# Performance work log

Measured on AMD Instinct MI355X. Metric: run time of the kernel, lower is better.

## Reference

```python
import jax, jax.numpy as jnp
import numpy as np

B, L, D, DFF = 4, 4096, 1024, 4096
EPS = 1e-6

def _rmsnorm(x, w):
    return x * jax.lax.rsqrt(jnp.mean(x * x, axis=-1, keepdims=True) + EPS) * w

def setup_inputs() -> dict:
    key = jax.random.key(0)
    ks = jax.random.split(key, 16)
    s = 1.0 / np.sqrt(D)
    sf = 1.0 / np.sqrt(DFF)
    return {
        "x": jax.random.normal(ks[0], (B, L, D), jnp.float32),
        # QuasiLSTM gate linears, stored [in, out]; y = x @ W + b
        "w_forget": jax.random.normal(ks[1], (D, D), jnp.float32) * s,
        "b_forget": jnp.zeros((D,), jnp.float32),
        "w_input": jax.random.normal(ks[2], (D, D), jnp.float32) * s,
        "b_input": jnp.zeros((D,), jnp.float32),
        "w_igate": jax.random.normal(ks[3], (D, D), jnp.float32) * s,
        "b_igate": jnp.zeros((D,), jnp.float32),
        "w_ogate": jax.random.normal(ks[4], (D, D), jnp.float32) * s,
        "b_ogate": jnp.zeros((D,), jnp.float32),
        "h0": jax.random.normal(ks[5], (D,), jnp.float32),  # last_hidden_init
        "norm1_w": jnp.ones((D,), jnp.float32),
        "norm2_w": jnp.ones((D,), jnp.float32),
        # FFN SwiGLU
        "w_fc": jax.random.normal(ks[6], (D, DFF), jnp.float32) * s,
        "b_fc": jnp.zeros((DFF,), jnp.float32),
        "w_fc_act": jax.random.normal(ks[7], (D, DFF), jnp.float32) * s,
        "b_fc_act": jnp.zeros((DFF,), jnp.float32),
        "w_out": jax.random.normal(ks[8], (DFF, D), jnp.float32) * sf,
        "b_out": jnp.zeros((D,), jnp.float32),
    }

def reference(x, w_forget, b_forget, w_input, b_input, w_igate, b_igate,
              w_ogate, b_ogate, h0, norm1_w, norm2_w,
              w_fc, b_fc, w_fc_act, b_fc_act, w_out, b_out):
    # --- QuasiLSTM branch (pre-norm residual) ---
    x_res = x
    xn = _rmsnorm(x, norm1_w)                                   # [B,L,D]
    forget = jax.nn.sigmoid(xn @ w_forget + b_forget)           # a_t
    inp = jnp.tanh(xn @ w_input + b_input) * jax.nn.sigmoid(xn @ w_igate + b_igate)  # b_t
    # Linear recurrence h_t = a_t * h_{t-1} + b_t, h_0 = 0 (inner chunk),
    # computed as an associative scan over the length axis.
    def comb(left, right):
        a_l, b_l = left
        a_r, b_r = right
        return (a_l * a_r, b_l * a_r + b_r)
    _, h_inner = jax.lax.associative_scan(comb, (forget, inp), axis=1)
    # cross-chunk contribution from last_hidden_init
    h = h_inner + h0[None, None, :] * jnp.cumprod(forget, axis=1)
    y = jnp.tanh(h) * jax.nn.sigmoid(xn @ w_ogate + b_ogate)
    x1 = y + x_res  # dropout p=0 -> identity
    # --- FFN SwiGLU branch ---
    xn2 = _rmsnorm(x1, norm2_w)
    hff = (xn2 @ w_fc + b_fc) * jax.nn.silu(xn2 @ w_fc_act + b_fc_act)
    out = hff @ w_out + b_out
    return out + x1
```

## Files before the change

### kernel.cpp

```cpp
#include <hip/hip_runtime.h>
#include <math.h>
#include <stdint.h>

static constexpr int Bb  = 4;
static constexpr int Ll  = 4096;
static constexpr int Dd  = 1024;
static constexpr int DFF = 4096;
static constexpr int Mm  = Bb * Ll;
static constexpr int CH  = 64;
static constexpr int CS  = Ll / CH;
static constexpr float EPS = 1e-6f;

typedef __attribute__((ext_vector_type(8))) short short8;
typedef __attribute__((ext_vector_type(4))) float floatx4;
typedef __attribute__((ext_vector_type(4))) unsigned short us4;

__device__ __forceinline__ float sigmoidf_(float v) { return 1.0f / (1.0f + __expf(-v)); }
__device__ __forceinline__ ushort f2bf(float f) {
    union { float f; uint32_t u; } v; v.f = f;
    return (ushort)((v.u + 0x7FFFu + ((v.u >> 16) & 1u)) >> 16);
}
__device__ __forceinline__ float bf2f(ushort h) {
    union { uint32_t u; float f; } v; v.u = (uint32_t)h << 16; return v.f;
}

__device__ __forceinline__ void gload16(const ushort* g, ushort* l) {
    __builtin_amdgcn_global_load_lds(
        (const __attribute__((address_space(1))) uint32_t*)g,
        (__attribute__((address_space(3))) uint32_t*)l, 16, 0, 0);
}

__device__ __forceinline__ void stage128x32(const ushort* __restrict__ src, int ld,
                                            int r0, int k0, ushort* lds, int tid)
{
    #pragma unroll
    for (int h = 0; h < 2; ++h) {
        int c  = tid + h * 256;
        int m  = c >> 2;
        int kb = (c & 3) ^ ((m >> 1) & 3);
        gload16(src + (size_t)(r0 + m) * ld + k0 + kb * 8, lds + c * 8);
    }
}

__global__ __launch_bounds__(256, 2) void mfma_gemm_sigmoid(
    const ushort* __restrict__ A, const ushort* __restrict__ Wt,
    const float* __restrict__ bias, ushort* __restrict__ C,
    int K, int ldC)
{
    __shared__ ushort As[128 * 32];
    __shared__ ushort Bs[128 * 32];
    int tid = threadIdx.x;
    int m0 = blockIdx.y * 128, n0 = blockIdx.x * 128;
    int wave = tid >> 6, lane = tid & 63;
    int wm = (wave >> 1) * 64, wn = (wave & 1) * 64;
    int fr = lane & 15, q = lane >> 4;
    int sw = (q ^ ((fr >> 1) & 3)) * 8;

    floatx4 acc[4][4] = {};

    for (int k0 = 0; k0 < K; k0 += 32) {
        stage128x32(A,  K, m0, k0, As, tid);
        stage128x32(Wt, K, n0, k0, Bs, tid);
        __syncthreads();
        short8 a[4], b[4];
        #pragma unroll
        for (int mi = 0; mi < 4; ++mi)
            a[mi] = *(const short8*)&As[(wm + mi * 16 + fr) * 32 + sw];
        #pragma unroll
        for (int ni = 0; ni < 4; ++ni)
            b[ni] = *(const short8*)&Bs[(wn + ni * 16 + fr) * 32 + sw];
        #pragma unroll
        for (int mi = 0; mi < 4; ++mi)
            #pragma unroll
            for (int ni = 0; ni < 4; ++ni)
                acc[mi][ni] = __builtin_amdgcn_mfma_f32_16x16x32_bf16(
                    a[mi], b[ni], acc[mi][ni], 0, 0, 0);
        __syncthreads();
    }

    #pragma unroll
    for (int ni = 0; ni < 4; ++ni) {
        int col = n0 + wn + ni * 16 + fr;
        float bsv = bias[col];
        #pragma unroll
        for (int mi = 0; mi < 4; ++mi)
            #pragma unroll
            for (int r = 0; r < 4; ++r) {
                int row = m0 + wm + mi * 16 + q * 4 + r;
                C[(size_t)row * ldC + col] = f2bf(sigmoidf_(acc[mi][ni][r] + bsv));
            }
    }
}

__global__ __launch_bounds__(256, 2) void mfma_gemm_dual(
    const ushort* __restrict__ A, const ushort* __restrict__ W1t,
    const float* __restrict__ b1, const ushort* __restrict__ W2t,
    const float* __restrict__ b2, ushort* __restrict__ C,
    int K, int ldC, int mode)
{
    __shared__ ushort As[128 * 32];
    __shared__ ushort B1s[128 * 32];
    __shared__ ushort B2s[128 * 32];
    int tid = threadIdx.x;
    int m0 = blockIdx.y * 128, n0 = blockIdx.x * 128;
    int wave = tid >> 6, lane = tid & 63;
    int wm = (wave >> 1) * 64, wn = (wave & 1) * 64;
    int fr = lane & 15, q = lane >> 4;
    int sw = (q ^ ((fr >> 1) & 3)) * 8;

    floatx4 acc1[4][4] = {};
    floatx4 acc2[4][4] = {};

    for (int k0 = 0; k0 < K; k0 += 32) {
        stage128x32(A,   K, m0, k0, As,  tid);
        stage128x32(W1t, K, n0, k0, B1s, tid);
        stage128x32(W2t, K, n0, k0, B2s, tid);
        __syncthreads();
        short8 a[4], b[4], c[4];
        #pragma unroll
        for (int mi = 0; mi < 4; ++mi)
            a[mi] = *(const short8*)&As[(wm + mi * 16 + fr) * 32 + sw];
        #pragma unroll
        for (int ni = 0; ni < 4; ++ni) {
            b[ni] = *(const short8*)&B1s[(wn + ni * 16 + fr) * 32 + sw];
            c[ni] = *(const short8*)&B2s[(wn + ni * 16 + fr) * 32 + sw];
        }
        #pragma unroll
        for (int mi = 0; mi < 4; ++mi)
            #pragma unroll
            for (int ni = 0; ni < 4; ++ni) {
                acc1[mi][ni] = __builtin_amdgcn_mfma_f32_16x16x32_bf16(
                    a[mi], b[ni], acc1[mi][ni], 0, 0, 0);
                acc2[mi][ni] = __builtin_amdgcn_mfma_f32_16x16x32_bf16(
                    a[mi], c[ni], acc2[mi][ni], 0, 0, 0);
            }
        __syncthreads();
    }

    #pragma unroll
    for (int ni = 0; ni < 4; ++ni) {
        int col = n0 + wn + ni * 16 + fr;
        float b1v = b1[col], b2v = b2[col];
        #pragma unroll
        for (int mi = 0; mi < 4; ++mi)
            #pragma unroll
            for (int r = 0; r < 4; ++r) {
                int row = m0 + wm + mi * 16 + q * 4 + r;
                float z1 = acc1[mi][ni][r] + b1v;
                float z2 = acc2[mi][ni][r] + b2v;
                float v = (mode == 0) ? tanhf(z1) * sigmoidf_(z2)
                                      : z1 * z2 * sigmoidf_(z2);
                C[(size_t)row * ldC + col] = f2bf(v);
            }
    }
}

__global__ __launch_bounds__(256, 2) void mfma_gemm_residual(
    const ushort* __restrict__ A, const ushort* __restrict__ Wt,
    const float* __restrict__ bias, float* __restrict__ C,
    int K, int ldC)
{
    __shared__ ushort As[128 * 32];
    __shared__ ushort Bs[128 * 32];
    int tid = threadIdx.x;
    int m0 = blockIdx.y * 128, n0 = blockIdx.x * 128;
    int wave = tid >> 6, lane = tid & 63;
    int wm = (wave >> 1) * 64, wn = (wave & 1) * 64;
    int fr = lane & 15, q = lane >> 4;
    int sw = (q ^ ((fr >> 1) & 3)) * 8;

    floatx4 acc[4][4] = {};

    for (int k0 = 0; k0 < K; k0 += 32) {
        stage128x32(A,  K, m0, k0, As, tid);
        stage128x32(Wt, K, n0, k0, Bs, tid);
        __syncthreads();
        short8 a[4], b[4];
        #pragma unroll
        for (int mi = 0; mi < 4; ++mi)
            a[mi] = *(const short8*)&As[(wm + mi * 16 + fr) * 32 + sw];
        #pragma unroll
        for (int ni = 0; ni < 4; ++ni)
            b[ni] = *(const short8*)&Bs[(wn + ni * 16 + fr) * 32 + sw];
        #pragma unroll
        for (int mi = 0; mi < 4; ++mi)
            #pragma unroll
            for (int ni = 0; ni < 4; ++ni)
                acc[mi][ni] = __builtin_amdgcn_mfma_f32_16x16x32_bf16(
                    a[mi], b[ni], acc[mi][ni], 0, 0, 0);
        __syncthreads();
    }

    #pragma unroll
    for (int ni = 0; ni < 4; ++ni) {
        int col = n0 + wn + ni * 16 + fr;
        float bsv = bias[col];
        #pragma unroll
        for (int mi = 0; mi < 4; ++mi)
            #pragma unroll
            for (int r = 0; r < 4; ++r) {
                int row = m0 + wm + mi * 16 + q * 4 + r;
                size_t idx = (size_t)row * ldC + col;
                C[idx] = acc[mi][ni][r] + bsv + C[idx];
            }
    }
}

__global__ __launch_bounds__(256) void transpose_cast_kernel(
    const float* __restrict__ W, ushort* __restrict__ Wt, int K, int N)
{
    __shared__ float t[32][33];
    int lx = threadIdx.x & 31, ly = threadIdx.x >> 5;
    int n = blockIdx.x * 32 + lx;
    #pragma unroll
    for (int i = 0; i < 4; ++i) {
        int k = blockIdx.y * 32 + ly + i * 8;
        t[ly + i * 8][lx] = W[(size_t)k * N + n];
    }
    __syncthreads();
    int k2 = blockIdx.y * 32 + lx;
    #pragma unroll
    for (int i = 0; i < 4; ++i) {
        int n2 = blockIdx.x * 32 + ly + i * 8;
        Wt[(size_t)n2 * K + k2] = f2bf(t[lx][ly + i * 8]);
    }
}

__global__ __launch_bounds__(256) void rmsnorm_bf16_kernel(
    const float* __restrict__ x, const float* __restrict__ w,
    ushort* __restrict__ o)
{
    int row = blockIdx.x;
    int tid = threadIdx.x;
    float4 v = ((const float4*)(x + (size_t)row * Dd))[tid];
    float ss = v.x*v.x + v.y*v.y + v.z*v.z + v.w*v.w;
    #pragma unroll
    for (int off = 32; off > 0; off >>= 1) ss += __shfl_down(ss, off, 64);
    __shared__ float red[4];
    if ((tid & 63) == 0) red[tid >> 6] = ss;
    __syncthreads();
    float scale = rsqrtf((red[0] + red[1] + red[2] + red[3]) * (1.0f / Dd) + EPS);
    float4 wv = ((const float4*)w)[tid];
    us4 ov;
    ov.x = f2bf(v.x * scale * wv.x);
    ov.y = f2bf(v.y * scale * wv.y);
    ov.z = f2bf(v.z * scale * wv.z);
    ov.w = f2bf(v.w * scale * wv.w);
    *(us4*)&o[(size_t)row * Dd + tid * 4] = ov;
}

__global__ __launch_bounds__(256) void scan_pass1(
    const ushort* __restrict__ Ga, const ushort* __restrict__ Gb,
    float* __restrict__ P, float* __restrict__ Hend)
{
    int d = blockIdx.x * 256 + threadIdx.x;
    int c = blockIdx.y, b = blockIdx.z;
    size_t base = ((size_t)b * Ll + (size_t)c * CS) * Dd + d;
    float p = 1.0f, h = 0.0f;
    for (int t = 0; t < CS; ++t) {
        size_t i = base + (size_t)t * Dd;
        float aa = bf2f(Ga[i]);
        float bb = bf2f(Gb[i]);
        p *= aa;
        h = aa * h + bb;
    }
    size_t o = ((size_t)b * CH + c) * Dd + d;
    P[o] = p;
    Hend[o] = h;
}

__global__ __launch_bounds__(256) void scan_pass2(
    const float* __restrict__ P, const float* __restrict__ Hend,
    const float* __restrict__ h0, float* __restrict__ Carry)
{
    int idx = blockIdx.x * 256 + threadIdx.x;
    int b = idx / Dd, d = idx % Dd;
    float carry = h0[d];
    for (int c = 0; c < CH; ++c) {
        size_t o = ((size_t)b * CH + c) * Dd + d;
        Carry[o] = carry;
        carry = P[o] * carry + Hend[o];
    }
}

__global__ __launch_bounds__(256) void scan_pass3_fused(
    const ushort* __restrict__ Ga, const ushort* __restrict__ Gb,
    const ushort* __restrict__ Gog, const float* __restrict__ Carry,
    const float* __restrict__ x, float* __restrict__ x1)
{
    int d = blockIdx.x * 256 + threadIdx.x;
    int c = blockIdx.y, b = blockIdx.z;
    size_t base = ((size_t)b * Ll + (size_t)c * CS) * Dd + d;
    float h = Carry[((size_t)b * CH + c) * Dd + d];
    for (int t = 0; t < CS; ++t) {
        size_t i = base + (size_t)t * Dd;
        float aa = bf2f(Ga[i]);
        float bb = bf2f(Gb[i]);
        h = aa * h + bb;
        x1[i] = tanhf(h) * bf2f(Gog[i]) + x[i];
    }
}

extern "C" void kernel_launch(void* const* d_in, const int* in_sizes, int n_in,
                              void* d_out, int out_size, void* d_ws, size_t ws_size,
                              hipStream_t stream)
{
    const float* x        = (const float*)d_in[0];
    const float* w_forget = (const float*)d_in[1];
    const float* b_forget = (const float*)d_in[2];
    const float* w_input  = (const float*)d_in[3];
    const float* b_input  = (const float*)d_in[4];
    const float* w_igate  = (const float*)d_in[5];
    const float* b_igate  = (const float*)d_in[6];
    const float* w_ogate  = (const float*)d_in[7];
    const float* b_ogate  = (const float*)d_in[8];
    const float* h0       = (const float*)d_in[9];
    const float* norm1_w  = (const float*)d_in[10];
    const float* norm2_w  = (const float*)d_in[11];
    const float* w_fc     = (const float*)d_in[12];
    const float* b_fc     = (const float*)d_in[13];
    const float* w_fc_act = (const float*)d_in[14];
    const float* b_fc_act = (const float*)d_in[15];
    const float* w_out    = (const float*)d_in[16];
    const float* b_out    = (const float*)d_in[17];
    float* out = (float*)d_out;

    char* ws = (char*)d_ws;
    const size_t MB = 1ull << 20;
    ushort* wtF   = (ushort*)(ws + 0 * MB);
    ushort* wtI   = (ushort*)(ws + 2 * MB);
    ushort* wtG   = (ushort*)(ws + 4 * MB);
    ushort* wtO   = (ushort*)(ws + 6 * MB);
    ushort* wtFC  = (ushort*)(ws + 8 * MB);
    ushort* wtFCA = (ushort*)(ws + 16 * MB);
    ushort* wtOUT = (ushort*)(ws + 24 * MB);
    ushort* xnb   = (ushort*)(ws + 32 * MB);
    ushort* Ga    = (ushort*)(ws + 64 * MB);
    ushort* Gb    = (ushort*)(ws + 96 * MB);
    ushort* Gog   = (ushort*)(ws + 128 * MB);
    ushort* hff   = (ushort*)(ws + 64 * MB);
    float*  P     = (float*)(ws + 192 * MB);
    float*  Hend  = (float*)(ws + 193 * MB);
    float*  Carry = (float*)(ws + 194 * MB);

    transpose_cast_kernel<<<dim3(Dd/32, Dd/32), 256, 0, stream>>>(w_forget, wtF,  Dd, Dd);
    transpose_cast_kernel<<<dim3(Dd/32, Dd/32), 256, 0, stream>>>(w_input,  wtI,  Dd, Dd);
    transpose_cast_kernel<<<dim3(Dd/32, Dd/32), 256, 0, stream>>>(w_igate,  wtG,  Dd, Dd);
    transpose_cast_kernel<<<dim3(Dd/32, Dd/32), 256, 0, stream>>>(w_ogate,  wtO,  Dd, Dd);
    transpose_cast_kernel<<<dim3(DFF/32, Dd/32), 256, 0, stream>>>(w_fc,     wtFC,  Dd, DFF);
    transpose_cast_kernel<<<dim3(DFF/32, Dd/32), 256, 0, stream>>>(w_fc_act, wtFCA, Dd, DFF);
    transpose_cast_kernel<<<dim3(Dd/32, DFF/32), 256, 0, stream>>>(w_out,    wtOUT, DFF, Dd);

    rmsnorm_bf16_kernel<<<Mm, 256, 0, stream>>>(x, norm1_w, xnb);

    dim3 gg(Dd / 128, Mm / 128);
    mfma_gemm_sigmoid<<<gg, 256, 0, stream>>>(xnb, wtF, b_forget, Ga, Dd, Dd);
    mfma_gemm_dual<<<gg, 256, 0, stream>>>(xnb, wtI, b_input, wtG, b_igate,
                                           Gb, Dd, Dd, 0);
    mfma_gemm_sigmoid<<<gg, 256, 0, stream>>>(xnb, wtO, b_ogate, Gog, Dd, Dd);

    dim3 sg(Dd / 256, CH, Bb);
    scan_pass1<<<sg, 256, 0, stream>>>(Ga, Gb, P, Hend);
    scan_pass2<<<(Bb * Dd) / 256, 256, 0, stream>>>(P, Hend, h0, Carry);
    scan_pass3_fused<<<sg, 256, 0, stream>>>(Ga, Gb, Gog, Carry, x, out);

    rmsnorm_bf16_kernel<<<Mm, 256, 0, stream>>>(out, norm2_w, xnb);

    dim3 gf(DFF / 128, Mm / 128);
    mfma_gemm_dual<<<gf, 256, 0, stream>>>(xnb, wtFC, b_fc, wtFCA, b_fc_act,
                                           hff, Dd, DFF, 1);

    dim3 go(Dd / 128, Mm / 128);
    mfma_gemm_residual<<<go, 256, 0, stream>>>(hff, wtOUT, b_out, out, DFF, Dd);
}
```

Measured before the change: 1.022 ms.

## Merge gate GEMMs into one dual GEMM and fuse second RMSNorm into scan

The four gate projections now run as a single dual-B GEMM over 2048 output columns: [input|forget] against [igate|ogate]. The epilogue branches by column to write Gb, Ga and Gog. The scan passes switch to one block per chunk covering the full model dimension with 4-wide vector loads, and the final scan pass also computes the second RMSNorm through a block reduction, which removes a separate norm kernel and a reread of x1. tanhf is replaced with an exp-based fast tanh, and the four gate weight transposes are merged into one launch. The trade-offs are fewer blocks in the scan kernels, two barriers per timestep in pass 3, and slightly lower accuracy from the fast tanh.

```diff
diff --git a/kernel.cpp b/kernel.cpp
--- a/kernel.cpp
+++ b/kernel.cpp
@@ -16,6 +16,9 @@
 typedef __attribute__((ext_vector_type(4))) unsigned short us4;
 
 __device__ __forceinline__ float sigmoidf_(float v) { return 1.0f / (1.0f + __expf(-v)); }
+__device__ __forceinline__ float fast_tanh(float x) {
+    return 2.0f / (1.0f + __expf(-2.0f * x)) - 1.0f;
+}
 __device__ __forceinline__ ushort f2bf(float f) {
     union { float f; uint32_t u; } v; v.f = f;
     return (ushort)((v.u + 0x7FFFu + ((v.u >> 16) & 1u)) >> 16);
@@ -42,61 +45,13 @@
     }
 }
 
-__global__ __launch_bounds__(256, 2) void mfma_gemm_sigmoid(
-    const ushort* __restrict__ A, const ushort* __restrict__ Wt,
-    const float* __restrict__ bias, ushort* __restrict__ C,
-    int K, int ldC)
-{
-    __shared__ ushort As[128 * 32];
-    __shared__ ushort Bs[128 * 32];
-    int tid = threadIdx.x;
-    int m0 = blockIdx.y * 128, n0 = blockIdx.x * 128;
-    int wave = tid >> 6, lane = tid & 63;
-    int wm = (wave >> 1) * 64, wn = (wave & 1) * 64;
-    int fr = lane & 15, q = lane >> 4;
-    int sw = (q ^ ((fr >> 1) & 3)) * 8;
-
-    floatx4 acc[4][4] = {};
-
-    for (int k0 = 0; k0 < K; k0 += 32) {
-        stage128x32(A,  K, m0, k0, As, tid);
-        stage128x32(Wt, K, n0, k0, Bs, tid);
-        __syncthreads();
-        short8 a[4], b[4];
-        #pragma unroll
-        for (int mi = 0; mi < 4; ++mi)
-            a[mi] = *(const short8*)&As[(wm + mi * 16 + fr) * 32 + sw];
-        #pragma unroll
-        for (int ni = 0; ni < 4; ++ni)
-            b[ni] = *(const short8*)&Bs[(wn + ni * 16 + fr) * 32 + sw];
-        #pragma unroll
-        for (int mi = 0; mi < 4; ++mi)
-            #pragma unroll
-            for (int ni = 0; ni < 4; ++ni)
-                acc[mi][ni] = __builtin_amdgcn_mfma_f32_16x16x32_bf16(
-                    a[mi], b[ni], acc[mi][ni], 0, 0, 0);
-        __syncthreads();
-    }
-
-    #pragma unroll
-    for (int ni = 0; ni < 4; ++ni) {
-        int col = n0 + wn + ni * 16 + fr;
-        float bsv = bias[col];
-        #pragma unroll
-        for (int mi = 0; mi < 4; ++mi)
-            #pragma unroll
-            for (int r = 0; r < 4; ++r) {
-                int row = m0 + wm + mi * 16 + q * 4 + r;
-                C[(size_t)row * ldC + col] = f2bf(sigmoidf_(acc[mi][ni][r] + bsv));
-            }
-    }
-}
-
-__global__ __launch_bounds__(256, 2) void mfma_gemm_dual(
+__global__ __launch_bounds__(256, 2) void mfma_gemm_gates(
     const ushort* __restrict__ A, const ushort* __restrict__ W1t,
-    const float* __restrict__ b1, const ushort* __restrict__ W2t,
-    const float* __restrict__ b2, ushort* __restrict__ C,
-    int K, int ldC, int mode)
+    const ushort* __restrict__ W2t,
+    const float* __restrict__ b_input, const float* __restrict__ b_forget,
+    const float* __restrict__ b_igate, const float* __restrict__ b_ogate,
+    ushort* __restrict__ Ga, ushort* __restrict__ Gb, ushort* __restrict__ Gog,
+    int K)
 {
     __shared__ ushort As[128 * 32];
     __shared__ ushort B1s[128 * 32];
@@ -140,28 +95,43 @@
     #pragma unroll
     for (int ni = 0; ni < 4; ++ni) {
         int col = n0 + wn + ni * 16 + fr;
-        float b1v = b1[col], b2v = b2[col];
-        #pragma unroll
-        for (int mi = 0; mi < 4; ++mi)
-            #pragma unroll
-            for (int r = 0; r < 4; ++r) {
-                int row = m0 + wm + mi * 16 + q * 4 + r;
-                float z1 = acc1[mi][ni][r] + b1v;
-                float z2 = acc2[mi][ni][r] + b2v;
-                float v = (mode == 0) ? tanhf(z1) * sigmoidf_(z2)
-                                      : z1 * z2 * sigmoidf_(z2);
-                C[(size_t)row * ldC + col] = f2bf(v);
-            }
-    }
-}
-
-__global__ __launch_bounds__(256, 2) void mfma_gemm_residual(
-    const ushort* __restrict__ A, const ushort* __restrict__ Wt,
-    const float* __restrict__ bias, float* __restrict__ C,
+        if (col < 1024) {
+            float b1v = b_input[col], b2v = b_igate[col];
+            #pragma unroll
+            for (int mi = 0; mi < 4; ++mi)
+                #pragma unroll
+                for (int r = 0; r < 4; ++r) {
+                    int row = m0 + wm + mi * 16 + q * 4 + r;
+                    float z1 = acc1[mi][ni][r] + b1v;
+                    float z2 = acc2[mi][ni][r] + b2v;
+                    Gb[(size_t)row * Dd + col] = f2bf(fast_tanh(z1) * sigmoidf_(z2));
+                }
+        } else {
+            int c2 = col - 1024;
+            float b1v = b_forget[c2], b2v = b_ogate[c2];
+            #pragma unroll
+            for (int mi = 0; mi < 4; ++mi)
+                #pragma unroll
+                for (int r = 0; r < 4; ++r) {
+                    int row = m0 + wm + mi * 16 + q * 4 + r;
+                    float z1 = acc1[mi][ni][r] + b1v;
+                    float z2 = acc2[mi][ni][r] + b2v;
+                    Ga[(size_t)row * Dd + c2]  = f2bf(sigmoidf_(z1));
+                    Gog[(size_t)row * Dd + c2] = f2bf(sigmoidf_(z2));
+                }
+        }
+    }
+}
+
+__global__ __launch_bounds__(256, 2) void mfma_gemm_swiglu(
+    const ushort* __restrict__ A, const ushort* __restrict__ W1t,
+    const float* __restrict__ b1, const ushort* __restrict__ W2t,
+    const float* __restrict__ b2, ushort* __restrict__ C,
     int K, int ldC)
 {
     __shared__ ushort As[128 * 32];
-    __shared__ ushort Bs[128 * 32];
+    __shared__ ushort B1s[128 * 32];
+    __shared__ ushort B2s[128 * 32];
     int tid = threadIdx.x;
     int m0 = blockIdx.y * 128, n0 = blockIdx.x * 128;
     int wave = tid >> 6, lane = tid & 63;
@@ -169,6 +139,65 @@
     int fr = lane & 15, q = lane >> 4;
     int sw = (q ^ ((fr >> 1) & 3)) * 8;
 
+    floatx4 acc1[4][4] = {};
+    floatx4 acc2[4][4] = {};
+
+    for (int k0 = 0; k0 < K; k0 += 32) {
+        stage128x32(A,   K, m0, k0, As,  tid);
+        stage128x32(W1t, K, n0, k0, B1s, tid);
+        stage128x32(W2t, K, n0, k0, B2s, tid);
+        __syncthreads();
+        short8 a[4], b[4], c[4];
+        #pragma unroll
+        for (int mi = 0; mi < 4; ++mi)
+            a[mi] = *(const short8*)&As[(wm + mi * 16 + fr) * 32 + sw];
+        #pragma unroll
+        for (int ni = 0; ni < 4; ++ni) {
+            b[ni] = *(const short8*)&B1s[(wn + ni * 16 + fr) * 32 + sw];
+            c[ni] = *(const short8*)&B2s[(wn + ni * 16 + fr) * 32 + sw];
+        }
+        #pragma unroll
+        for (int mi = 0; mi < 4; ++mi)
+            #pragma unroll
+            for (int ni = 0; ni < 4; ++ni) {
+                acc1[mi][ni] = __builtin_amdgcn_mfma_f32_16x16x32_bf16(
+                    a[mi], b[ni], acc1[mi][ni], 0, 0, 0);
+                acc2[mi][ni] = __builtin_amdgcn_mfma_f32_16x16x32_bf16(
+                    a[mi], c[ni], acc2[mi][ni], 0, 0, 0);
+            }
+        __syncthreads();
+    }
+
+    #pragma unroll
+    for (int ni = 0; ni < 4; ++ni) {
+        int col = n0 + wn + ni * 16 + fr;
+        float b1v = b1[col], b2v = b2[col];
+        #pragma unroll
+        for (int mi = 0; mi < 4; ++mi)
+            #pragma unroll
+            for (int r = 0; r < 4; ++r) {
+                int row = m0 + wm + mi * 16 + q * 4 + r;
+                float z1 = acc1[mi][ni][r] + b1v;
+                float z2 = acc2[mi][ni][r] + b2v;
+                C[(size_t)row * ldC + col] = f2bf(z1 * z2 * sigmoidf_(z2));
+            }
+    }
+}
+
+__global__ __launch_bounds__(256, 2) void mfma_gemm_residual(
+    const ushort* __restrict__ A, const ushort* __restrict__ Wt,
+    const float* __restrict__ bias, float* __restrict__ C,
+    int K, int ldC)
+{
+    __shared__ ushort As[128 * 32];
+    __shared__ ushort Bs[128 * 32];
+    int tid = threadIdx.x;
+    int m0 = blockIdx.y * 128, n0 = blockIdx.x * 128;
+    int wave = tid >> 6, lane = tid & 63;
+    int wm = (wave >> 1) * 64, wn = (wave & 1) * 64;
+    int fr = lane & 15, q = lane >> 4;
+    int sw = (q ^ ((fr >> 1) & 3)) * 8;
+
     floatx4 acc[4][4] = {};
 
     for (int k0 = 0; k0 < K; k0 += 32) {
@@ -223,6 +252,32 @@
     for (int i = 0; i < 4; ++i) {
         int n2 = blockIdx.x * 32 + ly + i * 8;
         Wt[(size_t)n2 * K + k2] = f2bf(t[lx][ly + i * 8]);
+    }
+}
+
+__global__ __launch_bounds__(256) void transpose_cast_gates(
+    const float* __restrict__ w_i, const float* __restrict__ w_f,
+    const float* __restrict__ w_g, const float* __restrict__ w_o,
+    ushort* __restrict__ W1t, ushort* __restrict__ W2t)
+{
+    int z = blockIdx.z;
+    const float* W = (z == 0) ? w_i : (z == 1) ? w_f : (z == 2) ? w_g : w_o;
+    ushort* Wt = (z == 0) ? W1t : (z == 1) ? W1t + (size_t)1024 * Dd
+               : (z == 2) ? W2t : W2t + (size_t)1024 * Dd;
+    __shared__ float t[32][33];
+    int lx = threadIdx.x & 31, ly = threadIdx.x >> 5;
+    int n = blockIdx.x * 32 + lx;
+    #pragma unroll
+    for (int i = 0; i < 4; ++i) {
+        int k = blockIdx.y * 32 + ly + i * 8;
+        t[ly + i * 8][lx] = W[(size_t)k * Dd + n];
+    }
+    __syncthreads();
+    int k2 = blockIdx.y * 32 + lx;
+    #pragma unroll
+    for (int i = 0; i < 4; ++i) {
+        int n2 = blockIdx.x * 32 + ly + i * 8;
+        Wt[(size_t)n2 * Dd + k2] = f2bf(t[lx][ly + i * 8]);
     }
 }
 
@@ -253,20 +308,26 @@
     const ushort* __restrict__ Ga, const ushort* __restrict__ Gb,
     float* __restrict__ P, float* __restrict__ Hend)
 {
-    int d = blockIdx.x * 256 + threadIdx.x;
-    int c = blockIdx.y, b = blockIdx.z;
-    size_t base = ((size_t)b * Ll + (size_t)c * CS) * Dd + d;
-    float p = 1.0f, h = 0.0f;
+    int tid = threadIdx.x;
+    int c = blockIdx.x, b = blockIdx.y;
+    size_t base = ((size_t)b * Ll + (size_t)c * CS) * Dd + tid * 4;
+    float p[4] = {1.f, 1.f, 1.f, 1.f};
+    float h[4] = {};
+    #pragma unroll 4
     for (int t = 0; t < CS; ++t) {
-        size_t i = base + (size_t)t * Dd;
-        float aa = bf2f(Ga[i]);
-        float bb = bf2f(Gb[i]);
-        p *= aa;
-        h = aa * h + bb;
-    }
-    size_t o = ((size_t)b * CH + c) * Dd + d;
-    P[o] = p;
-    Hend[o] = h;
+        us4 av = *(const us4*)&Ga[base + (size_t)t * Dd];
+        us4 bv = *(const us4*)&Gb[base + (size_t)t * Dd];
+        #pragma unroll
+        for (int j = 0; j < 4; ++j) {
+            float aa = bf2f(av[j]);
+            float bb = bf2f(bv[j]);
+            p[j] *= aa;
+            h[j] = aa * h[j] + bb;
+        }
+    }
+    size_t o = ((size_t)b * CH + c) * Dd + tid * 4;
+    *(float4*)&P[o]    = make_float4(p[0], p[1], p[2], p[3]);
+    *(float4*)&Hend[o] = make_float4(h[0], h[1], h[2], h[3]);
 }
 
 __global__ __launch_bounds__(256) void scan_pass2(
@@ -283,21 +344,48 @@
     }
 }
 
-__global__ __launch_bounds__(256) void scan_pass3_fused(
+__global__ __launch_bounds__(256) void scan_pass3_norm(
     const ushort* __restrict__ Ga, const ushort* __restrict__ Gb,
     const ushort* __restrict__ Gog, const float* __restrict__ Carry,
-    const float* __restrict__ x, float* __restrict__ x1)
-{
-    int d = blockIdx.x * 256 + threadIdx.x;
-    int c = blockIdx.y, b = blockIdx.z;
-    size_t base = ((size_t)b * Ll + (size_t)c * CS) * Dd + d;
-    float h = Carry[((size_t)b * CH + c) * Dd + d];
+    const float* __restrict__ x, const float* __restrict__ norm2w,
+    float* __restrict__ x1, ushort* __restrict__ xnb)
+{
+    int tid = threadIdx.x;
+    int c = blockIdx.x, b = blockIdx.y;
+    size_t base = ((size_t)b * Ll + (size_t)c * CS) * Dd + tid * 4;
+    float4 h4 = *(const float4*)&Carry[((size_t)b * CH + c) * Dd + tid * 4];
+    float h[4] = {h4.x, h4.y, h4.z, h4.w};
+    float4 w4 = ((const float4*)norm2w)[tid];
+    float wv[4] = {w4.x, w4.y, w4.z, w4.w};
+    __shared__ float red[4];
+
     for (int t = 0; t < CS; ++t) {
         size_t i = base + (size_t)t * Dd;
-        float aa = bf2f(Ga[i]);
-        float bb = bf2f(Gb[i]);
-        h = aa * h + bb;
-        x1[i] = tanhf(h) * bf2f(Gog[i]) + x[i];
+        us4 av = *(const us4*)&Ga[i];
+        us4 bv = *(const us4*)&Gb[i];
+        us4 gv = *(const us4*)&Gog[i];
+        float4 xv = *(const float4*)&x[i];
+        float xs[4] = {xv.x, xv.y, xv.z, xv.w};
+        float v[4];
+        #pragma unroll
+        for (int j = 0; j < 4; ++j) {
+            float aa = bf2f(av[j]);
+            float bb = bf2f(bv[j]);
+            h[j] = aa * h[j] + bb;
+            v[j] = fast_tanh(h[j]) * bf2f(gv[j]) + xs[j];
+        }
+        *(float4*)&x1[i] = make_float4(v[0], v[1], v[2], v[3]);
+        float ss = v[0]*v[0] + v[1]*v[1] + v[2]*v[2] + v[3]*v[3];
+        #pragma unroll
+        for (int off = 32; off > 0; off >>= 1) ss += __shfl_down(ss, off, 64);
+        if ((tid & 63) == 0) red[tid >> 6] = ss;
+        __syncthreads();
+        float scale = rsqrtf((red[0] + red[1] + red[2] + red[3]) * (1.0f / Dd) + EPS);
+        us4 ov;
+        #pragma unroll
+        for (int j = 0; j < 4; ++j) ov[j] = f2bf(v[j] * scale * wv[j]);
+        *(us4*)&xnb[i] = ov;
+        __syncthreads();
     }
 }
 
@@ -327,10 +415,8 @@
 
     char* ws = (char*)d_ws;
     const size_t MB = 1ull << 20;
-    ushort* wtF   = (ushort*)(ws + 0 * MB);
-    ushort* wtI   = (ushort*)(ws + 2 * MB);
-    ushort* wtG   = (ushort*)(ws + 4 * MB);
-    ushort* wtO   = (ushort*)(ws + 6 * MB);
+    ushort* wtG1  = (ushort*)(ws + 0 * MB);
+    ushort* wtG2  = (ushort*)(ws + 4 * MB);
     ushort* wtFC  = (ushort*)(ws + 8 * MB);
     ushort* wtFCA = (ushort*)(ws + 16 * MB);
     ushort* wtOUT = (ushort*)(ws + 24 * MB);
@@ -343,32 +429,28 @@
     float*  Hend  = (float*)(ws + 193 * MB);
     float*  Carry = (float*)(ws + 194 * MB);
 
-    transpose_cast_kernel<<<dim3(Dd/32, Dd/32), 256, 0, stream>>>(w_forget, wtF,  Dd, Dd);
-    transpose_cast_kernel<<<dim3(Dd/32, Dd/32), 256, 0, stream>>>(w_input,  wtI,  Dd, Dd);
-    transpose_cast_kernel<<<dim3(Dd/32, Dd/32), 256, 0, stream>>>(w_igate,  wtG,  Dd, Dd);
-    transpose_cast_kernel<<<dim3(Dd/32, Dd/32), 256, 0, stream>>>(w_ogate,  wtO,  Dd, Dd);
+    transpose_cast_gates<<<dim3(32, 32, 4), 256, 0, stream>>>(
+        w_input, w_forget, w_igate, w_ogate, wtG1, wtG2);
     transpose_cast_kernel<<<dim3(DFF/32, Dd/32), 256, 0, stream>>>(w_fc,     wtFC,  Dd, DFF);
     transpose_cast_kernel<<<dim3(DFF/32, Dd/32), 256, 0, stream>>>(w_fc_act, wtFCA, Dd, DFF);
     transpose_cast_kernel<<<dim3(Dd/32, DFF/32), 256, 0, stream>>>(w_out,    wtOUT, DFF, Dd);
 
     rmsnorm_bf16_kernel<<<Mm, 256, 0, stream>>>(x, norm1_w, xnb);
 
-    dim3 gg(Dd / 128, Mm / 128);
-    mfma_gemm_sigmoid<<<gg, 256, 0, stream>>>(xnb, wtF, b_forget, Ga, Dd, Dd);
-    mfma_gemm_dual<<<gg, 256, 0, stream>>>(xnb, wtI, b_input, wtG, b_igate,
-                                           Gb, Dd, Dd, 0);
-    mfma_gemm_sigmoid<<<gg, 256, 0, stream>>>(xnb, wtO, b_ogate, Gog, Dd, Dd);
-
-    dim3 sg(Dd / 256, CH, Bb);
+    dim3 gg(2048 / 128, Mm / 128);
+    mfma_gemm_gates<<<gg, 256, 0, stream>>>(xnb, wtG1, wtG2,
+                                            b_input, b_forget, b_igate, b_ogate,
+                                            Ga, Gb, Gog, Dd);
+
+    dim3 sg(CH, Bb);
     scan_pass1<<<sg, 256, 0, stream>>>(Ga, Gb, P, Hend);
     scan_pass2<<<(Bb * Dd) / 256, 256, 0, stream>>>(P, Hend, h0, Carry);
-    scan_pass3_fused<<<sg, 256, 0, stream>>>(Ga, Gb, Gog, Carry, x, out);
-
-    rmsnorm_bf16_kernel<<<Mm, 256, 0, stream>>>(out, norm2_w, xnb);
+    scan_pass3_norm<<<sg, 256, 0, stream>>>(Ga, Gb, Gog, Carry, x, norm2_w,
+                                            out, xnb);
 
     dim3 gf(DFF / 128, Mm / 128);
-    mfma_gemm_dual<<<gf, 256, 0, stream>>>(xnb, wtFC, b_fc, wtFCA, b_fc_act,
-                                           hff, Dd, DFF, 1);
+    mfma_gemm_swiglu<<<gf, 256, 0, stream>>>(xnb, wtFC, b_fc, wtFCA, b_fc_act,
+                                             hff, Dd, DFF);
 
     dim3 go(Dd / 128, Mm / 128);
     mfma_gemm_residual<<<go, 256, 0, stream>>>(hff, wtOUT, b_out, out, DFF, Dd);
```

Result: faster. 972.0 us (-4.9%).
